# Kernel optimization log

Measured on AMD Instinct MI355X. Metric: run time of the kernel, lower is better.

## Reference

```python
import jax, jax.numpy as jnp
import numpy as np

N_NODES = 50000
N_EDGES = 200000
NODE_F = 64
EDGE_F = 16
HID = 32
LAT = 16


def _glorot(key, shape):
    fan_in, fan_out = shape[0], shape[1]
    lim = np.sqrt(6.0 / (fan_in + fan_out))
    return jax.random.uniform(key, shape, jnp.float32, -lim, lim)


def setup_inputs() -> dict:
    key = jax.random.key(0)
    ks = jax.random.split(key, 24)
    inp = {
        "x": jax.random.normal(ks[0], (N_NODES, NODE_F), jnp.float32),
        "edge_index": jax.random.randint(ks[1], (2, N_EDGES), 0, N_NODES, jnp.int64),
        "edge_attr": jax.random.normal(ks[2], (N_EDGES, EDGE_F), jnp.float32),
        # encoder input projection
        "lin_in_w": _glorot(ks[3], (NODE_F, HID)),
        "lin_in_b": jnp.zeros((HID,), jnp.float32),
        # 3 edge MLPs (stacked over layer axis)
        "edge_w1": jnp.stack([_glorot(ks[4 + i], (EDGE_F, HID)) for i in range(3)]),
        "edge_b1": jnp.zeros((3, HID), jnp.float32),
        "edge_w2": jnp.stack([_glorot(ks[7 + i], (HID, HID * HID)) * 0.1 for i in range(3)]),
        "edge_b2": jnp.zeros((3, HID * HID), jnp.float32),
        # 3 NNConv root weights + biases
        "root_w": jnp.stack([_glorot(ks[10 + i], (HID, HID)) for i in range(3)]),
        "root_b": jnp.zeros((3, HID), jnp.float32),
        # encoder output projection
        "lin_out_w": _glorot(ks[13], (HID, LAT)),
        "lin_out_b": jnp.zeros((LAT,), jnp.float32),
        # node decoder MLP
        "dec_w1": _glorot(ks[14], (LAT, HID)),
        "dec_b1": jnp.zeros((HID,), jnp.float32),
        "dec_w2": _glorot(ks[15], (HID, NODE_F)),
        "dec_b2": jnp.zeros((NODE_F,), jnp.float32),
    }
    return inp


def _nnconv(x, src, dst, edge_attr, w1, b1, w2, b2, root_w, root_b):
    # per-edge weight matrix from edge MLP: [E, H, H]
    h = jax.nn.relu(edge_attr @ w1 + b1)
    w_e = (h @ w2 + b2).reshape(-1, HID, HID)
    # gather source features, per-edge matmul: [E, H]
    msg = jnp.einsum("eh,eho->eo", x[src], w_e)
    # scatter-mean to destinations
    agg = jax.ops.segment_sum(msg, dst, num_segments=N_NODES)
    cnt = jax.ops.segment_sum(jnp.ones((msg.shape[0], 1), x.dtype), dst, num_segments=N_NODES)
    agg = agg / jnp.maximum(cnt, 1.0)
    # root weight + bias
    return agg + x @ root_w + root_b


def reference(x, edge_index, edge_attr, lin_in_w, lin_in_b, edge_w1, edge_b1,
              edge_w2, edge_b2, root_w, root_b, lin_out_w, lin_out_b,
              dec_w1, dec_b1, dec_w2, dec_b2):
    src, dst = edge_index[0], edge_index[1]
    h = jax.nn.relu(x @ lin_in_w + lin_in_b)
    for i in range(3):  # fixed number of conv layers (dropout is identity in eval)
        h = _nnconv(h, src, dst, edge_attr, edge_w1[i], edge_b1[i],
                    edge_w2[i], edge_b2[i], root_w[i], root_b[i])
        h = jax.nn.relu(h)
    z = h @ lin_out_w + lin_out_b
    # node decoder
    d = jax.nn.relu(z @ dec_w1 + dec_b1)
    return d @ dec_w2 + dec_b2
```

## Files before the change

kernel.cpp:

```cpp
#include <hip/hip_runtime.h>
#include <hip/hip_bf16.h>
#include <stdint.h>

#define N_NODES 50000
#define N_EDGES 200000
#define NODE_F 64
#define EDGE_F 16
#define HID 32
#define LAT 16
#define KTOT 1056
#define SCAN_BLOCKS 196

typedef __attribute__((ext_vector_type(8))) short short8;
typedef __attribute__((ext_vector_type(4))) float f32x4;
typedef __attribute__((ext_vector_type(2))) float f32x2;

static __device__ __forceinline__ unsigned short bfbits(float f) {
  union { __hip_bfloat16 h; unsigned short s; } c; c.h = __float2bfloat16(f); return c.s;
}
static __device__ __forceinline__ unsigned pkt(f32x2 v) {
  return __builtin_amdgcn_perm(__float_as_uint(v.y), __float_as_uint(v.x), 0x07060302u);
}
union AFrag { short8 v; unsigned u[4]; };

__global__ void k_prep(const float* __restrict__ ew2, const float* __restrict__ eb2,
                       const float* __restrict__ ew1,
                       unsigned short* __restrict__ w2t,
                       unsigned short* __restrict__ w1p,
                       int* __restrict__ deg) {
  int g = blockIdx.x*256 + threadIdx.x;
  int l = g / (HID*KTOT);
  int r = g % (HID*KTOT);
  int o = r / KTOT;
  int kg = r % KTOT;
  int k = kg >> 5, h = kg & 31;
  float v = (k < 32) ? ew2[(size_t)l*32768 + k*1024 + h*32 + o]
                     : eb2[(size_t)l*1024 + h*32 + o];
  w2t[g] = bfbits(v);
  if (g < N_NODES) deg[g] = 0;
  if (g < 3*2*64*8) {
    int l2 = g >> 10;
    int r2 = g & 1023;
    int nt = r2 >> 9;
    int ln = (r2 >> 3) & 63;
    int j  = r2 & 7;
    int kgr = ln >> 4;
    float w = (kgr < 2) ? ew1[(size_t)l2*512 + (kgr*8 + j)*32 + nt*16 + (ln & 15)] : 0.f;
    w1p[g] = bfbits(w);
  }
}

__global__ void k_hist(const int* __restrict__ ei, int* __restrict__ deg) {
  int t = blockIdx.x*256 + threadIdx.x;
  if (t >= N_EDGES) return;
  int d = ei[N_EDGES + t];
  d = min(max(d, 0), N_NODES-1);
  atomicAdd(&deg[d], 1);
}

__global__ __launch_bounds__(256) void k_scan1(const int* __restrict__ deg,
                                               int* __restrict__ off,
                                               int* __restrict__ bsum) {
  __shared__ int s[256];
  const int tid = threadIdx.x;
  const int t = blockIdx.x*256 + tid;
  int d = (t < N_NODES) ? deg[t] : 0;
  s[tid] = d; __syncthreads();
  int v = d;
  #pragma unroll
  for (int ofs = 1; ofs < 256; ofs <<= 1) {
    int w = (tid >= ofs) ? s[tid-ofs] : 0;
    __syncthreads();
    v += w; s[tid] = v;
    __syncthreads();
  }
  if (t < N_NODES) off[t] = v - d;
  if (tid == 255) bsum[blockIdx.x] = v;
}

__global__ __launch_bounds__(256) void k_scan2(int* __restrict__ bsum) {
  __shared__ int s[256];
  const int tid = threadIdx.x;
  int d = (tid < SCAN_BLOCKS) ? bsum[tid] : 0;
  s[tid] = d; __syncthreads();
  int v = d;
  #pragma unroll
  for (int ofs = 1; ofs < 256; ofs <<= 1) {
    int w = (tid >= ofs) ? s[tid-ofs] : 0;
    __syncthreads();
    v += w; s[tid] = v;
    __syncthreads();
  }
  if (tid < SCAN_BLOCKS) bsum[tid] = v - d;
}

__global__ void k_scan3(int* __restrict__ off, const int* __restrict__ bsum,
                        int* __restrict__ cursor) {
  int t = blockIdx.x*256 + threadIdx.x;
  if (t < N_NODES) {
    off[t] += bsum[t >> 8];
    cursor[t] = 0;
  }
  if (t == 0) off[N_NODES] = N_EDGES;
}

__global__ void k_scatter(const int* __restrict__ ei, const int* __restrict__ off,
                          int* __restrict__ cursor, int* __restrict__ elist,
                          int* __restrict__ csr_pos) {
  int t = blockIdx.x*256 + threadIdx.x;
  if (t >= N_EDGES) return;
  int d = ei[N_EDGES + t];
  d = min(max(d, 0), N_NODES-1);
  int pos = atomicAdd(&cursor[d], 1);
  int slot = off[d] + pos;
  elist[slot] = t;
  csr_pos[t] = slot;
}

__global__ void k_lin_in(const float* __restrict__ x,
                         const float* __restrict__ W,
                         const float* __restrict__ b,
                         float* __restrict__ h) {
  __shared__ float Ws[NODE_F*HID];
  __shared__ float bs[HID];
  for (int i = threadIdx.x; i < NODE_F*HID; i += 256) Ws[i] = W[i];
  if (threadIdx.x < HID) bs[threadIdx.x] = b[threadIdx.x];
  __syncthreads();
  int t = blockIdx.x*256 + threadIdx.x;
  if (t >= N_NODES*HID) return;
  int n = t >> 5, o = t & 31;
  const float4* xp = (const float4*)(x + (size_t)n*NODE_F);
  float acc = bs[o];
  #pragma unroll
  for (int j = 0; j < NODE_F/4; j++) {
    float4 v = xp[j];
    acc = fmaf(v.x, Ws[(4*j+0)*HID+o], acc);
    acc = fmaf(v.y, Ws[(4*j+1)*HID+o], acc);
    acc = fmaf(v.z, Ws[(4*j+2)*HID+o], acc);
    acc = fmaf(v.w, Ws[(4*j+3)*HID+o], acc);
  }
  h[t] = fmaxf(acc, 0.f);
}

__global__ __launch_bounds__(256) void k_msg(const float* __restrict__ hin,
                                             const float* __restrict__ ea,
                                             const int* __restrict__ ei,
                                             const unsigned short* __restrict__ w1pl,
                                             const float* __restrict__ b1,
                                             const unsigned short* __restrict__ w2tl,
                                             const int* __restrict__ csr_pos,
                                             float* __restrict__ msgS) {
  __shared__ float sHE[256*33];
  __shared__ int   sSRC[256];
  __shared__ int   sPOS[256];
  const int tid = threadIdx.x;
  const int be  = blockIdx.x*256;
  const int wv   = tid >> 6;
  const int lane = tid & 63;
  const int nn   = lane & 15;
  const int quad = lane >> 4;
  const int wbase = wv*64;

  {
    int el = wbase + lane;
    int e = min(be + el, N_EDGES-1);
    sSRC[el] = min(max(ei[e], 0), N_NODES-1);
    sPOS[el] = csr_pos[e];
    sHE[el*33 + 32] = 1.0f;
  }

  {
    short8 wb0 = *(const short8*)(w1pl + lane*8);
    short8 wb1 = *(const short8*)(w1pl + 512 + lane*8);
    f32x4 z = {0.f,0.f,0.f,0.f};
    float bv0 = b1[nn], bv1 = b1[nn + 16];
    #pragma unroll
    for (int t = 0; t < 4; t++) {
      AFrag a;
      if (quad < 2) {
        int e = min(be + wbase + t*16 + nn, N_EDGES-1);
        const float4* p = (const float4*)(ea + (size_t)e*EDGE_F + quad*8);
        float4 u = p[0], v = p[1];
        a.u[0] = pkt(f32x2{u.x,u.y}); a.u[1] = pkt(f32x2{u.z,u.w});
        a.u[2] = pkt(f32x2{v.x,v.y}); a.u[3] = pkt(f32x2{v.z,v.w});
      } else {
        #pragma unroll
        for (int i = 0; i < 4; i++) a.u[i] = 0u;
      }
      f32x4 h0 = __builtin_amdgcn_mfma_f32_16x16x32_bf16(a.v, wb0, z, 0, 0, 0);
      f32x4 h1 = __builtin_amdgcn_mfma_f32_16x16x32_bf16(a.v, wb1, z, 0, 0, 0);
      #pragma unroll
      for (int r = 0; r < 4; r++) {
        int ro = (wbase + t*16 + quad*4 + r)*33;
        sHE[ro + nn]      = fmaxf(h0[r] + bv0, 0.f);
        sHE[ro + 16 + nn] = fmaxf(h1[r] + bv1, 0.f);
      }
    }
  }

  f32x2 xs[4][4];
  #pragma unroll
  for (int t = 0; t < 4; t++) {
    int si = sSRC[wbase + t*16 + nn];
    const float4* p = (const float4*)(hin + (size_t)si*HID);
    float4 a = p[quad*2], b = p[quad*2+1];
    xs[t][0] = f32x2{a.x, a.y}; xs[t][1] = f32x2{a.z, a.w};
    xs[t][2] = f32x2{b.x, b.y}; xs[t][3] = f32x2{b.z, b.w};
  }

  f32x4 c0[4], c1[4];
  #pragma unroll
  for (int t = 0; t < 4; t++) { c0[t] = f32x4{0.f,0.f,0.f,0.f}; c1[t] = c0[t]; }

  const unsigned short* bp0 = w2tl + (unsigned)nn*KTOT + quad*8;
  const unsigned short* bp1 = bp0 + 16*KTOT;
  const float* heR[4];
  #pragma unroll
  for (int t = 0; t < 4; t++) heR[t] = sHE + (wbase + t*16 + nn)*33;

  short8 sb0[3], sb1[3];
  float  sh[3][4];
  #pragma unroll
  for (int j = 0; j < 3; j++) {
    sb0[j] = *(const short8*)(bp0 + j*32);
    sb1[j] = *(const short8*)(bp1 + j*32);
    #pragma unroll
    for (int t = 0; t < 4; t++) sh[j][t] = heR[t][j];
  }

  #pragma unroll 1
  for (int base = 0; base < 30; base += 3) {
    #pragma unroll
    for (int j = 0; j < 3; j++) {
      const int kk = base + j;
      short8 cb0 = sb0[j], cb1 = sb1[j];
      #pragma unroll
      for (int t = 0; t < 4; t++) {
        float hk = sh[j][t];
        AFrag a;
        #pragma unroll
        for (int i = 0; i < 4; i++) a.u[i] = pkt(xs[t][i]*hk);
        c0[t] = __builtin_amdgcn_mfma_f32_16x16x32_bf16(a.v, cb0, c0[t], 0, 0, 0);
        c1[t] = __builtin_amdgcn_mfma_f32_16x16x32_bf16(a.v, cb1, c1[t], 0, 0, 0);
      }
      sb0[j] = *(const short8*)(bp0 + (kk+3)*32);
      sb1[j] = *(const short8*)(bp1 + (kk+3)*32);
      #pragma unroll
      for (int t = 0; t < 4; t++) sh[j][t] = heR[t][kk+3];
    }
  }
  #pragma unroll
  for (int j = 0; j < 3; j++) {
    short8 cb0 = sb0[j], cb1 = sb1[j];
    #pragma unroll
    for (int t = 0; t < 4; t++) {
      float hk = sh[j][t];
      AFrag a;
      #pragma unroll
      for (int i = 0; i < 4; i++) a.u[i] = pkt(xs[t][i]*hk);
      c0[t] = __builtin_amdgcn_mfma_f32_16x16x32_bf16(a.v, cb0, c0[t], 0, 0, 0);
      c1[t] = __builtin_amdgcn_mfma_f32_16x16x32_bf16(a.v, cb1, c1[t], 0, 0, 0);
    }
  }

  #pragma unroll
  for (int t = 0; t < 4; t++) {
    #pragma unroll
    for (int r = 0; r < 4; r++) {
      int el = wbase + t*16 + quad*4 + r;
      if (be + el < N_EDGES) {
        size_t row = (size_t)sPOS[el]*HID;
        msgS[row +      nn] = c0[t][r];
        msgS[row + 16 + nn] = c1[t][r];
      }
    }
  }
}

__global__ void k_gather(const float* __restrict__ msgS,
                         const int* __restrict__ off,
                         const float* __restrict__ hin,
                         const float* __restrict__ rw,
                         const float* __restrict__ rb,
                         float* __restrict__ hout) {
  __shared__ float rws[HID*HID];
  __shared__ float rbs[HID];
  for (int i = threadIdx.x; i < HID*HID; i += 256) rws[i] = rw[i];
  if (threadIdx.x < HID) rbs[threadIdx.x] = rb[threadIdx.x];
  __syncthreads();
  int t = blockIdx.x*256 + threadIdx.x;
  if (t >= N_NODES*8) return;
  int n = t >> 3, oc = t & 7;
  int s0 = off[n], s1 = off[n+1];
  float a0 = 0.f, a1 = 0.f, a2 = 0.f, a3 = 0.f;
  for (int j = s0; j < s1; j++) {
    float4 v = ((const float4*)(msgS + (size_t)j*HID))[oc];
    a0 += v.x; a1 += v.y; a2 += v.z; a3 += v.w;
  }
  float inv = 1.f / fmaxf((float)(s1 - s0), 1.f);
  a0 = fmaf(a0, inv, rbs[oc*4+0]);
  a1 = fmaf(a1, inv, rbs[oc*4+1]);
  a2 = fmaf(a2, inv, rbs[oc*4+2]);
  a3 = fmaf(a3, inv, rbs[oc*4+3]);
  const float4* hp = (const float4*)(hin + (size_t)n*HID);
  #pragma unroll
  for (int jq = 0; jq < 8; jq++) {
    float4 hv = hp[jq];
    #pragma unroll
    for (int c = 0; c < 4; c++) {
      int j = jq*4 + c;
      float h = (c==0)?hv.x:(c==1)?hv.y:(c==2)?hv.z:hv.w;
      const float4* rp = (const float4*)(rws + j*HID + oc*4);
      float4 r = rp[0];
      a0 = fmaf(h, r.x, a0);
      a1 = fmaf(h, r.y, a1);
      a2 = fmaf(h, r.z, a2);
      a3 = fmaf(h, r.w, a3);
    }
  }
  float4 res = make_float4(fmaxf(a0,0.f), fmaxf(a1,0.f), fmaxf(a2,0.f), fmaxf(a3,0.f));
  ((float4*)(hout + (size_t)n*HID))[oc] = res;
}

__global__ void k_decoder(const float* __restrict__ h,
                          const float* __restrict__ lo_w, const float* __restrict__ lo_b,
                          const float* __restrict__ d1_w, const float* __restrict__ d1_b,
                          const float* __restrict__ d2_w, const float* __restrict__ d2_b,
                          float* __restrict__ out) {
  __shared__ float lows[HID*LAT], lobs[LAT], d1s[LAT*HID], d1bs[HID], d2s[HID*NODE_F], d2bs[NODE_F];
  for (int i = threadIdx.x; i < HID*LAT; i += 256) lows[i] = lo_w[i];
  for (int i = threadIdx.x; i < LAT; i += 256) lobs[i] = lo_b[i];
  for (int i = threadIdx.x; i < LAT*HID; i += 256) d1s[i] = d1_w[i];
  for (int i = threadIdx.x; i < HID; i += 256) d1bs[i] = d1_b[i];
  for (int i = threadIdx.x; i < HID*NODE_F; i += 256) d2s[i] = d2_w[i];
  for (int i = threadIdx.x; i < NODE_F; i += 256) d2bs[i] = d2_b[i];
  __syncthreads();
  int n = blockIdx.x*256 + threadIdx.x;
  if (n >= N_NODES) return;
  float hr[HID];
  const float4* hp = (const float4*)(h + (size_t)n*HID);
  #pragma unroll
  for (int i = 0; i < HID/4; i++) { float4 v = hp[i]; hr[4*i]=v.x; hr[4*i+1]=v.y; hr[4*i+2]=v.z; hr[4*i+3]=v.w; }
  float z[LAT];
  #pragma unroll
  for (int o = 0; o < LAT; o++) {
    float a = lobs[o];
    #pragma unroll
    for (int j = 0; j < HID; j++) a = fmaf(hr[j], lows[j*LAT+o], a);
    z[o] = a;
  }
  float d[HID];
  #pragma unroll
  for (int o = 0; o < HID; o++) {
    float a = d1bs[o];
    #pragma unroll
    for (int j = 0; j < LAT; j++) a = fmaf(z[j], d1s[j*HID+o], a);
    d[o] = fmaxf(a, 0.f);
  }
  float* op = out + (size_t)n*NODE_F;
  #pragma unroll 8
  for (int o = 0; o < NODE_F; o++) {
    float a = d2bs[o];
    #pragma unroll
    for (int j = 0; j < HID; j++) a = fmaf(d[j], d2s[j*NODE_F+o], a);
    op[o] = a;
  }
}

extern "C" void kernel_launch(void* const* d_in, const int* in_sizes, int n_in,
                              void* d_out, int out_size, void* d_ws, size_t ws_size,
                              hipStream_t stream) {
  const float* x   = (const float*)d_in[0];
  const int*   ei  = (const int*)d_in[1];
  const float* ea  = (const float*)d_in[2];
  const float* liw = (const float*)d_in[3];
  const float* lib = (const float*)d_in[4];
  const float* ew1 = (const float*)d_in[5];
  const float* eb1 = (const float*)d_in[6];
  const float* ew2 = (const float*)d_in[7];
  const float* eb2 = (const float*)d_in[8];
  const float* rw  = (const float*)d_in[9];
  const float* rb  = (const float*)d_in[10];
  const float* low = (const float*)d_in[11];
  const float* lob = (const float*)d_in[12];
  const float* d1w = (const float*)d_in[13];
  const float* d1b = (const float*)d_in[14];
  const float* d2w = (const float*)d_in[15];
  const float* d2b = (const float*)d_in[16];
  float* out = (float*)d_out;

  float* h0   = (float*)d_ws;
  float* h1   = h0  + (size_t)N_NODES*HID;
  float* msg  = h1  + (size_t)N_NODES*HID;
  int*  deg   = (int*)(msg + (size_t)N_EDGES*HID);
  int*  off   = deg + N_NODES;
  int*  cursor= off + N_NODES + 16;
  int*  elist = cursor + N_NODES;
  int*  cpos  = elist + N_EDGES;
  int*  bsum  = cpos + N_EDGES;
  unsigned short* w2t = (unsigned short*)(bsum + 256);
  unsigned short* w1p = w2t + 3*HID*KTOT;

  k_prep<<<(3*HID*KTOT)/256, 256, 0, stream>>>(ew2, eb2, ew1, w2t, w1p, deg);
  k_hist<<<(N_EDGES + 255)/256, 256, 0, stream>>>(ei, deg);
  k_scan1<<<SCAN_BLOCKS, 256, 0, stream>>>(deg, off, bsum);
  k_scan2<<<1, 256, 0, stream>>>(bsum);
  k_scan3<<<(N_NODES + 255)/256, 256, 0, stream>>>(off, bsum, cursor);
  k_scatter<<<(N_EDGES + 255)/256, 256, 0, stream>>>(ei, off, cursor, elist, cpos);

  k_lin_in<<<(N_NODES*HID + 255)/256, 256, 0, stream>>>(x, liw, lib, h0);

  float* hin = h0; float* hout = h1;
  for (int i = 0; i < 3; i++) {
    k_msg<<<(N_EDGES + 255)/256, 256, 0, stream>>>(hin, ea, ei,
        w1p + (size_t)i*1024, eb1 + i*HID,
        w2t + (size_t)i*HID*KTOT, cpos, msg);
    k_gather<<<(N_NODES*8 + 255)/256, 256, 0, stream>>>(msg, off, hin,
        rw + i*HID*HID, rb + i*HID, hout);
    float* t = hin; hin = hout; hout = t;
  }

  k_decoder<<<(N_NODES + 255)/256, 256, 0, stream>>>(hin, low, lob, d1w, d1b, d2w, d2b, out);
}
```

Measured before the change: 287.8 us.

## Split k_msg work across waves by N and K halves, store bf16 messages, fuse scans

k_msg now gives each 256-thread block 64 edges, with four waves splitting the output columns and the K dimension in halves. Partial sums are reduced through LDS, which raises the block count and cuts per-wave MFMA work. Messages are stored as bf16, halving the write and the k_gather read traffic at some precision cost. Separately, scan2 and scan3 are merged so each block sums the preceding block totals itself, and the unused elist output of the scatter is dropped.

```diff
diff --git a/kernel.cpp b/kernel.cpp
--- a/kernel.cpp
+++ b/kernel.cpp
@@ -78,43 +78,37 @@
   if (tid == 255) bsum[blockIdx.x] = v;
 }
 
-__global__ __launch_bounds__(256) void k_scan2(int* __restrict__ bsum) {
-  __shared__ int s[256];
+__global__ __launch_bounds__(256) void k_scan23(int* __restrict__ off,
+                                                const int* __restrict__ bsum,
+                                                int* __restrict__ cursor) {
+  __shared__ int sPref;
   const int tid = threadIdx.x;
-  int d = (tid < SCAN_BLOCKS) ? bsum[tid] : 0;
-  s[tid] = d; __syncthreads();
-  int v = d;
-  #pragma unroll
-  for (int ofs = 1; ofs < 256; ofs <<= 1) {
-    int w = (tid >= ofs) ? s[tid-ofs] : 0;
-    __syncthreads();
-    v += w; s[tid] = v;
-    __syncthreads();
-  }
-  if (tid < SCAN_BLOCKS) bsum[tid] = v - d;
-}
-
-__global__ void k_scan3(int* __restrict__ off, const int* __restrict__ bsum,
-                        int* __restrict__ cursor) {
-  int t = blockIdx.x*256 + threadIdx.x;
+  const int b = blockIdx.x;
+  if (tid < 64) {
+    int acc = 0;
+    for (int i = tid; i < b; i += 64) acc += bsum[i];
+    #pragma unroll
+    for (int o = 32; o; o >>= 1) acc += __shfl_down(acc, o);
+    if (tid == 0) sPref = acc;
+  }
+  __syncthreads();
+  int pref = sPref;
+  int t = b*256 + tid;
   if (t < N_NODES) {
-    off[t] += bsum[t >> 8];
+    off[t] += pref;
     cursor[t] = 0;
   }
   if (t == 0) off[N_NODES] = N_EDGES;
 }
 
 __global__ void k_scatter(const int* __restrict__ ei, const int* __restrict__ off,
-                          int* __restrict__ cursor, int* __restrict__ elist,
-                          int* __restrict__ csr_pos) {
+                          int* __restrict__ cursor, int* __restrict__ csr_pos) {
   int t = blockIdx.x*256 + threadIdx.x;
   if (t >= N_EDGES) return;
   int d = ei[N_EDGES + t];
   d = min(max(d, 0), N_NODES-1);
   int pos = atomicAdd(&cursor[d], 1);
-  int slot = off[d] + pos;
-  elist[slot] = t;
-  csr_pos[t] = slot;
+  csr_pos[t] = off[d] + pos;
 }
 
 __global__ void k_lin_in(const float* __restrict__ x,
@@ -149,36 +143,38 @@
                                              const float* __restrict__ b1,
                                              const unsigned short* __restrict__ w2tl,
                                              const int* __restrict__ csr_pos,
-                                             float* __restrict__ msgS) {
-  __shared__ float sHE[256*33];
-  __shared__ int   sSRC[256];
-  __shared__ int   sPOS[256];
+                                             unsigned short* __restrict__ msgB) {
+  __shared__ float sHE[64*33];
+  __shared__ float sRED[2*64*17];
+  __shared__ int   sSRC[64];
+  __shared__ int   sPOS[64];
   const int tid = threadIdx.x;
-  const int be  = blockIdx.x*256;
+  const int be  = blockIdx.x*64;
   const int wv   = tid >> 6;
   const int lane = tid & 63;
   const int nn   = lane & 15;
   const int quad = lane >> 4;
-  const int wbase = wv*64;
-
-  {
-    int el = wbase + lane;
-    int e = min(be + el, N_EDGES-1);
-    sSRC[el] = min(max(ei[e], 0), N_NODES-1);
-    sPOS[el] = csr_pos[e];
-    sHE[el*33 + 32] = 1.0f;
-  }
-
-  {
+  const int nhalf = wv & 1;
+  const int khalf = wv >> 1;
+
+  if (tid < 64) {
+    int e = be + tid;
+    sSRC[tid] = min(max(ei[e], 0), N_NODES-1);
+    sPOS[tid] = csr_pos[e];
+    sHE[tid*33 + 32] = 1.0f;
+  }
+
+  if (khalf == 0) {
     short8 wb0 = *(const short8*)(w1pl + lane*8);
     short8 wb1 = *(const short8*)(w1pl + 512 + lane*8);
     f32x4 z = {0.f,0.f,0.f,0.f};
     float bv0 = b1[nn], bv1 = b1[nn + 16];
     #pragma unroll
-    for (int t = 0; t < 4; t++) {
+    for (int ti = 0; ti < 2; ti++) {
+      int t = nhalf*2 + ti;
       AFrag a;
       if (quad < 2) {
-        int e = min(be + wbase + t*16 + nn, N_EDGES-1);
+        int e = be + t*16 + nn;
         const float4* p = (const float4*)(ea + (size_t)e*EDGE_F + quad*8);
         float4 u = p[0], v = p[1];
         a.u[0] = pkt(f32x2{u.x,u.y}); a.u[1] = pkt(f32x2{u.z,u.w});
@@ -191,93 +187,113 @@
       f32x4 h1 = __builtin_amdgcn_mfma_f32_16x16x32_bf16(a.v, wb1, z, 0, 0, 0);
       #pragma unroll
       for (int r = 0; r < 4; r++) {
-        int ro = (wbase + t*16 + quad*4 + r)*33;
+        int ro = (t*16 + quad*4 + r)*33;
         sHE[ro + nn]      = fmaxf(h0[r] + bv0, 0.f);
         sHE[ro + 16 + nn] = fmaxf(h1[r] + bv1, 0.f);
       }
     }
   }
+  __syncthreads();
 
   f32x2 xs[4][4];
   #pragma unroll
   for (int t = 0; t < 4; t++) {
-    int si = sSRC[wbase + t*16 + nn];
+    int si = sSRC[t*16 + nn];
     const float4* p = (const float4*)(hin + (size_t)si*HID);
     float4 a = p[quad*2], b = p[quad*2+1];
     xs[t][0] = f32x2{a.x, a.y}; xs[t][1] = f32x2{a.z, a.w};
     xs[t][2] = f32x2{b.x, b.y}; xs[t][3] = f32x2{b.z, b.w};
   }
 
-  f32x4 c0[4], c1[4];
-  #pragma unroll
-  for (int t = 0; t < 4; t++) { c0[t] = f32x4{0.f,0.f,0.f,0.f}; c1[t] = c0[t]; }
-
-  const unsigned short* bp0 = w2tl + (unsigned)nn*KTOT + quad*8;
-  const unsigned short* bp1 = bp0 + 16*KTOT;
+  f32x4 c[4];
+  #pragma unroll
+  for (int t = 0; t < 4; t++) c[t] = f32x4{0.f,0.f,0.f,0.f};
+
+  const int k0 = khalf*16;
+  const unsigned short* bp = w2tl + (unsigned)nn*KTOT + quad*8 + (unsigned)nhalf*(16*KTOT);
   const float* heR[4];
   #pragma unroll
-  for (int t = 0; t < 4; t++) heR[t] = sHE + (wbase + t*16 + nn)*33;
-
-  short8 sb0[3], sb1[3];
+  for (int t = 0; t < 4; t++) heR[t] = sHE + (t*16 + nn)*33;
+
+  short8 sb[3];
   float  sh[3][4];
   #pragma unroll
   for (int j = 0; j < 3; j++) {
-    sb0[j] = *(const short8*)(bp0 + j*32);
-    sb1[j] = *(const short8*)(bp1 + j*32);
-    #pragma unroll
-    for (int t = 0; t < 4; t++) sh[j][t] = heR[t][j];
+    int kk = k0 + j;
+    sb[j] = *(const short8*)(bp + kk*32);
+    #pragma unroll
+    for (int t = 0; t < 4; t++) sh[j][t] = heR[t][kk];
   }
 
   #pragma unroll 1
-  for (int base = 0; base < 30; base += 3) {
+  for (int base = 0; base < 15; base += 3) {
     #pragma unroll
     for (int j = 0; j < 3; j++) {
-      const int kk = base + j;
-      short8 cb0 = sb0[j], cb1 = sb1[j];
+      const int s = base + j;
+      short8 cb = sb[j];
       #pragma unroll
       for (int t = 0; t < 4; t++) {
         float hk = sh[j][t];
         AFrag a;
         #pragma unroll
         for (int i = 0; i < 4; i++) a.u[i] = pkt(xs[t][i]*hk);
-        c0[t] = __builtin_amdgcn_mfma_f32_16x16x32_bf16(a.v, cb0, c0[t], 0, 0, 0);
-        c1[t] = __builtin_amdgcn_mfma_f32_16x16x32_bf16(a.v, cb1, c1[t], 0, 0, 0);
+        c[t] = __builtin_amdgcn_mfma_f32_16x16x32_bf16(a.v, cb, c[t], 0, 0, 0);
       }
-      sb0[j] = *(const short8*)(bp0 + (kk+3)*32);
-      sb1[j] = *(const short8*)(bp1 + (kk+3)*32);
-      #pragma unroll
-      for (int t = 0; t < 4; t++) sh[j][t] = heR[t][kk+3];
-    }
-  }
-  #pragma unroll
-  for (int j = 0; j < 3; j++) {
-    short8 cb0 = sb0[j], cb1 = sb1[j];
+      int sn = s + 3;
+      int kkn = (sn >= 16) ? 32 : (k0 + sn);
+      sb[j] = *(const short8*)(bp + kkn*32);
+      #pragma unroll
+      for (int t = 0; t < 4; t++) sh[j][t] = heR[t][kkn];
+    }
+  }
+  {
+    short8 cb = sb[0];
     #pragma unroll
     for (int t = 0; t < 4; t++) {
-      float hk = sh[j][t];
+      float hk = sh[0][t];
       AFrag a;
       #pragma unroll
       for (int i = 0; i < 4; i++) a.u[i] = pkt(xs[t][i]*hk);
-      c0[t] = __builtin_amdgcn_mfma_f32_16x16x32_bf16(a.v, cb0, c0[t], 0, 0, 0);
-      c1[t] = __builtin_amdgcn_mfma_f32_16x16x32_bf16(a.v, cb1, c1[t], 0, 0, 0);
-    }
-  }
-
-  #pragma unroll
-  for (int t = 0; t < 4; t++) {
-    #pragma unroll
-    for (int r = 0; r < 4; r++) {
-      int el = wbase + t*16 + quad*4 + r;
-      if (be + el < N_EDGES) {
-        size_t row = (size_t)sPOS[el]*HID;
-        msgS[row +      nn] = c0[t][r];
-        msgS[row + 16 + nn] = c1[t][r];
+      c[t] = __builtin_amdgcn_mfma_f32_16x16x32_bf16(a.v, cb, c[t], 0, 0, 0);
+    }
+  }
+  if (khalf == 0) {
+    short8 cb = sb[1];
+    #pragma unroll
+    for (int t = 0; t < 4; t++) {
+      float hk = sh[1][t];
+      AFrag a;
+      #pragma unroll
+      for (int i = 0; i < 4; i++) a.u[i] = pkt(xs[t][i]*hk);
+      c[t] = __builtin_amdgcn_mfma_f32_16x16x32_bf16(a.v, cb, c[t], 0, 0, 0);
+    }
+  }
+
+  if (khalf == 1) {
+    #pragma unroll
+    for (int t = 0; t < 4; t++) {
+      #pragma unroll
+      for (int r = 0; r < 4; r++) {
+        int el = t*16 + quad*4 + r;
+        sRED[(nhalf*64 + el)*17 + nn] = c[t][r];
       }
     }
   }
-}
-
-__global__ void k_gather(const float* __restrict__ msgS,
+  __syncthreads();
+  if (khalf == 0) {
+    #pragma unroll
+    for (int t = 0; t < 4; t++) {
+      #pragma unroll
+      for (int r = 0; r < 4; r++) {
+        int el = t*16 + quad*4 + r;
+        float v = c[t][r] + sRED[(nhalf*64 + el)*17 + nn];
+        msgB[(size_t)sPOS[el]*HID + nhalf*16 + nn] = bfbits(v);
+      }
+    }
+  }
+}
+
+__global__ void k_gather(const unsigned short* __restrict__ msgB,
                          const int* __restrict__ off,
                          const float* __restrict__ hin,
                          const float* __restrict__ rw,
@@ -294,8 +310,11 @@
   int s0 = off[n], s1 = off[n+1];
   float a0 = 0.f, a1 = 0.f, a2 = 0.f, a3 = 0.f;
   for (int j = s0; j < s1; j++) {
-    float4 v = ((const float4*)(msgS + (size_t)j*HID))[oc];
-    a0 += v.x; a1 += v.y; a2 += v.z; a3 += v.w;
+    uint2 u = *(const uint2*)(msgB + (size_t)j*HID + oc*4);
+    a0 += __uint_as_float(u.x << 16);
+    a1 += __uint_as_float(u.x & 0xffff0000u);
+    a2 += __uint_as_float(u.y << 16);
+    a3 += __uint_as_float(u.y & 0xffff0000u);
   }
   float inv = 1.f / fmaxf((float)(s1 - s0), 1.f);
   a0 = fmaf(a0, inv, rbs[oc*4+0]);
@@ -391,12 +410,11 @@
 
   float* h0   = (float*)d_ws;
   float* h1   = h0  + (size_t)N_NODES*HID;
-  float* msg  = h1  + (size_t)N_NODES*HID;
-  int*  deg   = (int*)(msg + (size_t)N_EDGES*HID);
+  unsigned short* msgB = (unsigned short*)(h1 + (size_t)N_NODES*HID);
+  int*  deg   = (int*)(msgB + (size_t)N_EDGES*HID);
   int*  off   = deg + N_NODES;
   int*  cursor= off + N_NODES + 16;
-  int*  elist = cursor + N_NODES;
-  int*  cpos  = elist + N_EDGES;
+  int*  cpos  = cursor + N_NODES;
   int*  bsum  = cpos + N_EDGES;
   unsigned short* w2t = (unsigned short*)(bsum + 256);
   unsigned short* w1p = w2t + 3*HID*KTOT;
@@ -404,18 +422,17 @@
   k_prep<<<(3*HID*KTOT)/256, 256, 0, stream>>>(ew2, eb2, ew1, w2t, w1p, deg);
   k_hist<<<(N_EDGES + 255)/256, 256, 0, stream>>>(ei, deg);
   k_scan1<<<SCAN_BLOCKS, 256, 0, stream>>>(deg, off, bsum);
-  k_scan2<<<1, 256, 0, stream>>>(bsum);
-  k_scan3<<<(N_NODES + 255)/256, 256, 0, stream>>>(off, bsum, cursor);
-  k_scatter<<<(N_EDGES + 255)/256, 256, 0, stream>>>(ei, off, cursor, elist, cpos);
+  k_scan23<<<SCAN_BLOCKS, 256, 0, stream>>>(off, bsum, cursor);
+  k_scatter<<<(N_EDGES + 255)/256, 256, 0, stream>>>(ei, off, cursor, cpos);
 
   k_lin_in<<<(N_NODES*HID + 255)/256, 256, 0, stream>>>(x, liw, lib, h0);
 
   float* hin = h0; float* hout = h1;
   for (int i = 0; i < 3; i++) {
-    k_msg<<<(N_EDGES + 255)/256, 256, 0, stream>>>(hin, ea, ei,
+    k_msg<<<N_EDGES/64, 256, 0, stream>>>(hin, ea, ei,
         w1p + (size_t)i*1024, eb1 + i*HID,
-        w2t + (size_t)i*HID*KTOT, cpos, msg);
-    k_gather<<<(N_NODES*8 + 255)/256, 256, 0, stream>>>(msg, off, hin,
+        w2t + (size_t)i*HID*KTOT, cpos, msgB);
+    k_gather<<<(N_NODES*8 + 255)/256, 256, 0, stream>>>(msgB, off, hin,
         rw + i*HID*HID, rb + i*HID, hout);
     float* t = hin; hin = hout; hout = t;
   }
```

Result: slower. 305.7 us (+6.2%).
